# Kernel tuning notes

Hardware: AMD Instinct MI355X
Metric: run time of the kernel (lower is better)

The kernel has to match this reference:

```python
import jax, jax.numpy as jnp
import numpy as np

B, N = 2, 200
IMG = 2048
NC = 4                    # node concepts ('Is*')
NODE_CH = NC * 256        # 1024
EC = 3                    # edge concepts minus 'HigherPri'
AC = 4                    # actions
BBOX_MAX = 1024.0
E = N * (N - 1)

# static fully-connected directed edge list (src=i, dst=j, i!=j), row-major order
_ii, _jj = np.meshgrid(np.arange(N), np.arange(N), indexing='ij')
_m = _ii != _jj
SRC = jnp.asarray(_ii[_m])
DST = jnp.asarray(_jj[_m])


def _lin(k, fin, fout):
    kw, kb = jax.random.split(k)
    s = 1.0 / np.sqrt(fin)
    return (jax.random.uniform(kw, (fin, fout), jnp.float32, -s, s),
            jax.random.uniform(kb, (fout,), jnp.float32, -s, s))


def setup_inputs():
    ks = jax.random.split(jax.random.key(0), 16)
    p = {}
    p['roi_features'] = jax.random.normal(ks[0], (B, N, IMG), jnp.float32)
    p['batch_bboxes'] = jax.random.uniform(ks[1], (B, N, 4), jnp.float32) * BBOX_MAX
    p['batch_directions'] = jax.random.normal(ks[2], (B, N, 4), jnp.float32)
    p['batch_priorities'] = jax.random.normal(ks[3], (B, N), jnp.float32)
    p['w1'], p['b1'] = _lin(ks[4], IMG, 512)
    p['w2'], p['b2'] = _lin(ks[5], 512, 256)
    p['w3'], p['b3'] = _lin(ks[6], 256, NODE_CH)
    p['wi'], p['bi'] = _lin(ks[7], NODE_CH, NC)
    p['we1'], p['be1'] = _lin(ks[8], 16, 256)
    p['we2'], p['be2'] = _lin(ks[9], 256, 64)
    p['we3'], p['be3'] = _lin(ks[10], 64, EC)
    p['wp1'], p['bp1'] = _lin(ks[11], EC + 1, 128)
    p['wp2'], p['bp2'] = _lin(ks[12], 128, NODE_CH * AC)
    p['root_w'], _ = _lin(ks[13], NODE_CH, AC)
    _, p['root_b'] = _lin(ks[14], NODE_CH, AC)
    return p


def reference(roi_features, batch_bboxes, batch_directions, batch_priorities,
              w1, b1, w2, b2, w3, b3, wi, bi,
              we1, be1, we2, be2, we3, be3,
              wp1, bp1, wp2, bp2, root_w, root_b):
    # node concept embedding MLP: [B,N,IMG] -> [B,N,NODE_CH]
    h = jax.nn.relu(roi_features @ w1 + b1)
    h = jax.nn.relu(h @ w2 + b2)
    node_concepts = h @ w3 + b3
    node_concepts_explicit = jax.nn.sigmoid(node_concepts @ wi + bi)

    # pairwise attributes for all directed edges (same ordering as torch masks)
    node_attr = jnp.concatenate([batch_bboxes / BBOX_MAX, batch_directions], -1)  # [B,N,8]
    pair = jnp.concatenate([node_attr[:, SRC], node_attr[:, DST]], -1)            # [B,E,16]
    eh = jax.nn.relu(pair @ we1 + be1)
    eh = jax.nn.relu(eh @ we2 + be2)
    edge_attributes = jax.nn.sigmoid(eh @ we3 + be3)                              # [B,E,EC]
    higher_pri = (batch_priorities[:, SRC] > batch_priorities[:, DST]).astype(jnp.float32)
    edge_attributes = jnp.concatenate([edge_attributes, higher_pri[..., None]], -1)  # [B,E,EC+1]

    # NNConv on graph 0: per-edge weight matrix, gather-matmul-scatter
    x = node_concepts[0]                 # [N, NODE_CH]
    e = edge_attributes[0]               # [E, EC+1]
    w = jax.nn.relu(e @ wp1 + bp1) @ wp2 + bp2
    w = w.reshape(E, NODE_CH, AC)        # [E, NODE_CH, AC]
    msg = jnp.einsum('ei,eio->eo', x[SRC], w)          # [E, AC]
    agg = jax.ops.segment_sum(msg, DST, num_segments=N)  # [N, AC]
    next_actions = agg + x @ root_w + root_b
    return (next_actions, node_concepts_explicit[0], edge_attributes[0])
```

## Files before the change

kernel.cpp:

```cpp
#include <hip/hip_runtime.h>
#include <math.h>

#define NN 200
#define ETOT 39800

typedef float float4v __attribute__((ext_vector_type(4)));
typedef short short8 __attribute__((ext_vector_type(8)));

__device__ __forceinline__ float sigf(float x) { return 1.0f / (1.0f + expf(-x)); }

__device__ __forceinline__ unsigned short f2b(float f) {
  unsigned u = __float_as_uint(f);
  u += 0x7fffu + ((u >> 16) & 1u);
  return (unsigned short)(u >> 16);
}
__device__ __forceinline__ float b2f16(unsigned short u) {
  return __uint_as_float(((unsigned)u) << 16);
}

__global__ __launch_bounds__(256) void k_prep(
    const float* __restrict__ w1, const float* __restrict__ w2, const float* __restrict__ wp2,
    const float* __restrict__ w3, const float* __restrict__ wi, const float* __restrict__ rootw,
    const float* __restrict__ bp2, const float* __restrict__ b3, const float* __restrict__ we2,
    const float* __restrict__ bbox, const float* __restrict__ dir,
    const float* __restrict__ we1, const float* __restrict__ be1, const float* __restrict__ wp1,
    unsigned short* __restrict__ w1T, unsigned short* __restrict__ w2T,
    unsigned short* __restrict__ WrT, unsigned short* __restrict__ we2T,
    float* __restrict__ G12f, float* __restrict__ Pm, float* __restrict__ Qm,
    float* __restrict__ gvec, float* __restrict__ wp1T, float* __restrict__ bcat) {
  __shared__ __align__(16) char sm[16640];
  const int b = blockIdx.x, tid = threadIdx.x;
  const int lane = tid & 63, wv = tid >> 6;

  if (b < 288) {
    float (*lds)[65] = (float (*)[65])sm;
    const float* Wf;
    unsigned short* Wt;
    int K, N, t;
    if (b < 256) { Wf = w1; Wt = w1T; K = 2048; N = 512; t = b; }
    else { Wf = w2; Wt = w2T; K = 512; N = 256; t = b - 256; }
    const int K64 = K >> 6;
    const int kt = t % K64, nt = t / K64;
#pragma unroll 4
    for (int i = 0; i < 16; ++i) {
      int idx = tid + i * 256;
      int r = idx >> 6, c = idx & 63;
      lds[r][c] = Wf[(size_t)(kt * 64 + r) * N + nt * 64 + c];
    }
    __syncthreads();
#pragma unroll 4
    for (int i = 0; i < 16; ++i) {
      int idx = tid + i * 256;
      int r = idx >> 6, c = idx & 63;
      Wt[(size_t)(nt * 64 + r) * K + kt * 64 + c] = f2b(lds[c][r]);
    }
  } else if (b < 416) {
    int k = b - 288;
    int o = tid >> 6, l = tid & 63;
    const float* src = wp2 + (size_t)k * 4096;
    unsigned short* dst = WrT + (size_t)(k * 4 + o) * 1024;
    for (int i = l; i < 1024; i += 64) dst[i] = f2b(src[i * 4 + o]);
  } else if (b < 672) {
    const int c = b - 416;
    float s[12] = {};
#pragma unroll
    for (int ii = 0; ii < 4; ++ii) {
      int i = tid + ii * 256;
      float xv = w3[(size_t)c * 1024 + i];
      float4v wi4 = ((const float4v*)wi)[i];
      float4v rw4 = ((const float4v*)rootw)[i];
      float4v bp4 = ((const float4v*)bp2)[i];
#pragma unroll
      for (int q = 0; q < 4; ++q) {
        s[q] += xv * wi4[q]; s[4 + q] += xv * rw4[q]; s[8 + q] += xv * bp4[q];
      }
    }
    float (*part)[12] = (float (*)[12])sm;
#pragma unroll
    for (int r = 0; r < 12; ++r) {
      float v = s[r];
#pragma unroll
      for (int off = 32; off > 0; off >>= 1) v += __shfl_down(v, off, 64);
      if (lane == 0) part[wv][r] = v;
    }
    __syncthreads();
    if (tid < 12) G12f[c * 12 + tid] = part[0][tid] + part[1][tid] + part[2][tid] + part[3][tid];
  } else if (b < 872) {
    const int n = b - 672, c = tid;
    float a[8];
#pragma unroll
    for (int r = 0; r < 4; ++r) a[r] = bbox[n * 4 + r] * (1.0f / 1024.0f);
#pragma unroll
    for (int r = 0; r < 4; ++r) a[4 + r] = dir[n * 4 + r];
    float p = be1[c], q = 0.0f;
#pragma unroll
    for (int r = 0; r < 8; ++r) {
      p += a[r] * we1[r * 256 + c];
      q += a[r] * we1[(8 + r) * 256 + c];
    }
    Pm[n * 256 + c] = p;
    Qm[n * 256 + c] = q;
  } else if (b < 888) {
    const int f = (b - 872) * 256 + tid;
    const int c = f >> 6, k0 = (f & 63) * 4;
#pragma unroll
    for (int q = 0; q < 4; ++q)
      we2T[c * 256 + k0 + q] = f2b(we2[(k0 + q) * 64 + c]);
  } else if (b < 896) {
    const int j = (b - 888) * 64 + (tid >> 2), p = tid & 3;
    const float* src = wp2 + (size_t)(j >> 2) * 4096 + (j & 3);
    float v = 0.f;
    for (int t = 0; t < 256; ++t) {
      int i = p + 4 * t;
      v += b3[i] * src[4 * i];
    }
    v += __shfl_down(v, 2, 4);
    v += __shfl_down(v, 1, 4);
    if (p == 0) gvec[j] = v;
  } else if (b == 896) {
    if (tid < 128) {
      float4v v = {wp1[tid], wp1[128 + tid], wp1[256 + tid], wp1[384 + tid]};
      ((float4v*)wp1T)[tid] = v;
    }
  } else {
    float s[12] = {};
#pragma unroll
    for (int ii = 0; ii < 4; ++ii) {
      int i = tid + ii * 256;
      float xv = b3[i];
      float4v wi4 = ((const float4v*)wi)[i];
      float4v rw4 = ((const float4v*)rootw)[i];
      float4v bp4 = ((const float4v*)bp2)[i];
#pragma unroll
      for (int q = 0; q < 4; ++q) {
        s[q] += xv * wi4[q]; s[4 + q] += xv * rw4[q]; s[8 + q] += xv * bp4[q];
      }
    }
    float (*part)[12] = (float (*)[12])sm;
#pragma unroll
    for (int r = 0; r < 12; ++r) {
      float v = s[r];
#pragma unroll
      for (int off = 32; off > 0; off >>= 1) v += __shfl_down(v, off, 64);
      if (lane == 0) part[wv][r] = v;
    }
    __syncthreads();
    if (tid < 12) bcat[tid] = part[0][tid] + part[1][tid] + part[2][tid] + part[3][tid];
  }
}

__global__ __launch_bounds__(256) void k_mid(
    const float* __restrict__ roi, const unsigned short* __restrict__ w1T, const float* __restrict__ b1,
    const unsigned short* __restrict__ WrT, const float* __restrict__ w3,
    unsigned short* __restrict__ h1, unsigned short* __restrict__ Gm) {
  __shared__ float red[4][16][17];
  const int b = blockIdx.x, tid = threadIdx.x;
  const int lane = tid & 63, wv = tid >> 6, mr = lane & 15, quad = lane >> 4;

  if (b < 416) {
    const int m0 = (b % 13) * 16, n0 = (b / 13) * 16;
    const int arow = min(m0 + mr, 199);
    const float* Ap = roi + (size_t)arow * 2048 + wv * 512 + quad * 8;
    const unsigned short* Bp = w1T + (size_t)(n0 + mr) * 2048 + wv * 512 + quad * 8;
    float4v acc = {0.f, 0.f, 0.f, 0.f};
    for (int ks = 0; ks < 16; ++ks) {
      float4v a0 = *(const float4v*)(Ap + ks * 32);
      float4v a1 = *(const float4v*)(Ap + ks * 32 + 4);
      short8 af;
      af[0]=f2b(a0[0]); af[1]=f2b(a0[1]); af[2]=f2b(a0[2]); af[3]=f2b(a0[3]);
      af[4]=f2b(a1[0]); af[5]=f2b(a1[1]); af[6]=f2b(a1[2]); af[7]=f2b(a1[3]);
      short8 bf = *(const short8*)(Bp + ks * 32);
      acc = __builtin_amdgcn_mfma_f32_16x16x32_bf16(af, bf, acc, 0, 0, 0);
    }
#pragma unroll
    for (int r = 0; r < 4; ++r) red[wv][quad * 4 + r][mr] = acc[r];
    __syncthreads();
    const int row = tid >> 4, col = tid & 15;
    float v = red[0][row][col] + red[1][row][col] + red[2][row][col] + red[3][row][col] + b1[n0 + col];
    h1[(size_t)(m0 + row) * 512 + n0 + col] = f2b(fmaxf(v, 0.f));
  } else {
    const int t = b - 416;
    const int j0 = (t % 32) * 16, c0 = (t / 32) * 16;
    const unsigned short* Ap = WrT + (size_t)(j0 + mr) * 1024 + wv * 256 + quad * 8;
    const float* Bp = w3 + (size_t)(c0 + mr) * 1024 + wv * 256 + quad * 8;
    float4v acc = {0.f, 0.f, 0.f, 0.f};
    for (int ks = 0; ks < 8; ++ks) {
      short8 af = *(const short8*)(Ap + ks * 32);
      float4v b0 = *(const float4v*)(Bp + ks * 32);
      float4v b1v = *(const float4v*)(Bp + ks * 32 + 4);
      short8 bf;
      bf[0]=f2b(b0[0]); bf[1]=f2b(b0[1]); bf[2]=f2b(b0[2]); bf[3]=f2b(b0[3]);
      bf[4]=f2b(b1v[0]); bf[5]=f2b(b1v[1]); bf[6]=f2b(b1v[2]); bf[7]=f2b(b1v[3]);
      acc = __builtin_amdgcn_mfma_f32_16x16x32_bf16(af, bf, acc, 0, 0, 0);
    }
#pragma unroll
    for (int r = 0; r < 4; ++r) red[wv][quad * 4 + r][mr] = acc[r];
    __syncthreads();
    const int row = tid >> 4, col = tid & 15;
    float v = red[0][row][col] + red[1][row][col] + red[2][row][col] + red[3][row][col];
    Gm[(size_t)(j0 + row) * 256 + c0 + col] = f2b(v);
  }
}

__global__ __launch_bounds__(256) void k_h2(const unsigned short* __restrict__ h1,
                                            const unsigned short* __restrict__ w2T,
                                            const float* __restrict__ b2,
                                            unsigned short* __restrict__ h2) {
  __shared__ float red[4][16][17];
  const int tid = threadIdx.x, lane = tid & 63, wv = tid >> 6;
  const int m0 = (blockIdx.x % 13) * 16, n0 = (blockIdx.x / 13) * 16;
  const int mr = lane & 15, quad = lane >> 4;
  const unsigned short* Ap = h1 + (size_t)(m0 + mr) * 512 + wv * 128 + quad * 8;
  const unsigned short* Bp = w2T + (size_t)(n0 + mr) * 512 + wv * 128 + quad * 8;
  float4v acc = {0.f, 0.f, 0.f, 0.f};
#pragma unroll
  for (int s = 0; s < 4; ++s) {
    short8 af = *(const short8*)(Ap + s * 32);
    short8 bf = *(const short8*)(Bp + s * 32);
    acc = __builtin_amdgcn_mfma_f32_16x16x32_bf16(af, bf, acc, 0, 0, 0);
  }
#pragma unroll
  for (int r = 0; r < 4; ++r) red[wv][quad * 4 + r][mr] = acc[r];
  __syncthreads();
  const int row = tid >> 4, col = tid & 15;
  float v = red[0][row][col] + red[1][row][col] + red[2][row][col] + red[3][row][col] + b2[n0 + col];
  h2[(size_t)(m0 + row) * 256 + n0 + col] = f2b(fmaxf(v, 0.f));
}

__global__ __launch_bounds__(256) void k_TN(const unsigned short* __restrict__ h2,
                                            const unsigned short* __restrict__ Gm,
                                            const float* __restrict__ gvec,
                                            const float* __restrict__ G12f, const float* __restrict__ bcat,
                                            const float* __restrict__ bi, const float* __restrict__ rootb,
                                            float* __restrict__ Tm, float* __restrict__ out1,
                                            float* __restrict__ Um, float* __restrict__ out0) {
  __shared__ __align__(16) char sm[4352];
  const int b = blockIdx.x, tid = threadIdx.x;
  const int lane = tid & 63, wv = tid >> 6, mr = lane & 15, quad = lane >> 4;
  if (b < 416) {
    float (*red)[16][17] = (float (*)[16][17])sm;
    const int m0 = (b % 13) * 16, n0 = (b / 13) * 16;
    const unsigned short* Ap = h2 + (size_t)(m0 + mr) * 256 + wv * 64 + quad * 8;
    const unsigned short* Bp = Gm + (size_t)(n0 + mr) * 256 + wv * 64 + quad * 8;
    float4v acc = {0.f, 0.f, 0.f, 0.f};
#pragma unroll
    for (int s = 0; s < 2; ++s) {
      short8 af = *(const short8*)(Ap + s * 32);
      short8 bf = *(const short8*)(Bp + s * 32);
      acc = __builtin_amdgcn_mfma_f32_16x16x32_bf16(af, bf, acc, 0, 0, 0);
    }
#pragma unroll
    for (int r = 0; r < 4; ++r) red[wv][quad * 4 + r][mr] = acc[r];
    __syncthreads();
    const int row = tid >> 4, col = tid & 15;
    float v = red[0][row][col] + red[1][row][col] + red[2][row][col] + red[3][row][col] + gvec[n0 + col];
    Tm[(size_t)(m0 + row) * 512 + n0 + col] = v;
  } else {
    const int n = b - 416;
    const float xv = b2f16(h2[(size_t)n * 256 + tid]);
    const float4v* g4 = (const float4v*)(G12f + tid * 12);
    float s[12];
    float4v v0 = g4[0], v1 = g4[1], v2 = g4[2];
    s[0]=xv*v0[0]; s[1]=xv*v0[1]; s[2]=xv*v0[2]; s[3]=xv*v0[3];
    s[4]=xv*v1[0]; s[5]=xv*v1[1]; s[6]=xv*v1[2]; s[7]=xv*v1[3];
    s[8]=xv*v2[0]; s[9]=xv*v2[1]; s[10]=xv*v2[2]; s[11]=xv*v2[3];
    float (*part)[12] = (float (*)[12])sm;
#pragma unroll
    for (int r = 0; r < 12; ++r) {
      float v = s[r];
#pragma unroll
      for (int off = 32; off > 0; off >>= 1) v += __shfl_down(v, off, 64);
      if (lane == 0) part[wv][r] = v;
    }
    __syncthreads();
    if (tid < 12) {
      float v = part[0][tid] + part[1][tid] + part[2][tid] + part[3][tid] + bcat[tid];
      int kind = tid >> 2, c = tid & 3;
      if (kind == 0) out1[n * 4 + c] = sigf(v + bi[c]);
      else if (kind == 1) out0[n * 4 + c] = v + rootb[c];
      else Um[n * 4 + c] = v;
    }
  }
}

__global__ __launch_bounds__(256) void k_edge(
    const float* __restrict__ P, const float* __restrict__ Q,
    const unsigned short* __restrict__ we2T,
    const float* __restrict__ be2, const float* __restrict__ we3, const float* __restrict__ be3,
    const float* __restrict__ wp1T, const float* __restrict__ bp1,
    const float* __restrict__ pri,
    const float* __restrict__ T, const float* __restrict__ U,
    float* __restrict__ out0, float* __restrict__ out_ea) {
  __shared__ int src_s[64], dst_s[64];
  __shared__ float ea_s[64][4];
  __shared__ float4v wp1s[128];
  __shared__ float bp1s[128];
  __shared__ float4v Ts[2][128];
  __shared__ float Us[2][4];

  const int tid = threadIdx.x;
  const int e0 = blockIdx.x * 64;
  const int s_lo = e0 / 199;

  if (tid < 64) {
    int e = e0 + tid;
    int i = -1, j = 0;
    if (e < ETOT) {
      i = e / 199;
      int jj = e - i * 199;
      j = jj + (jj >= i ? 1 : 0);
    }
    src_s[tid] = i;
    dst_s[tid] = j;
  }
  if (tid < 128) {
    wp1s[tid] = ((const float4v*)wp1T)[tid];
    bp1s[tid] = bp1[tid];
  }
  {
    int row = tid >> 7, c = tid & 127;
    Ts[row][c] = ((const float4v*)T)[(s_lo + row) * 128 + c];
  }
  if (tid < 8) {
    int s = min(s_lo + (tid >> 2), 199);
    Us[tid >> 2][tid & 3] = U[s * 4 + (tid & 3)];
  }
  __syncthreads();

  const int lane = tid & 63;
  const int wv = tid >> 6;
  const int m = lane & 15;
  const int quad = lane >> 4;
  const int eloc = wv * 16 + m;
  const int si = src_s[eloc];
  const int dj = dst_s[eloc];

  float4v acc[4];
#pragma unroll
  for (int ct = 0; ct < 4; ++ct) { acc[ct][0] = 0.f; acc[ct][1] = 0.f; acc[ct][2] = 0.f; acc[ct][3] = 0.f; }

  const short8* W8 = (const short8*)we2T;

  for (int ks = 0; ks < 8; ++ks) {
    union { short8 s; unsigned u[4]; } af;
    af.s = (short8)0;
    if (si >= 0) {
      const float4v* p4 = (const float4v*)(P + si * 256 + ks * 32 + quad * 8);
      const float4v* q4 = (const float4v*)(Q + dj * 256 + ks * 32 + quad * 8);
      float4v v0 = p4[0] + q4[0];
      float4v v1 = p4[1] + q4[1];
      af.u[0] = (unsigned)f2b(fmaxf(v0[0], 0.f)) | ((unsigned)f2b(fmaxf(v0[1], 0.f)) << 16);
      af.u[1] = (unsigned)f2b(fmaxf(v0[2], 0.f)) | ((unsigned)f2b(fmaxf(v0[3], 0.f)) << 16);
      af.u[2] = (unsigned)f2b(fmaxf(v1[0], 0.f)) | ((unsigned)f2b(fmaxf(v1[1], 0.f)) << 16);
      af.u[3] = (unsigned)f2b(fmaxf(v1[2], 0.f)) | ((unsigned)f2b(fmaxf(v1[3], 0.f)) << 16);
    }
#pragma unroll
    for (int ct = 0; ct < 4; ++ct) {
      short8 bf = W8[(ct * 16 + m) * 32 + ks * 4 + quad];
      acc[ct] = __builtin_amdgcn_mfma_f32_16x16x32_bf16(af.s, bf, acc[ct], 0, 0, 0);
    }
  }

  float ev[4][3];
#pragma unroll
  for (int r = 0; r < 4; ++r) { ev[r][0] = 0.f; ev[r][1] = 0.f; ev[r][2] = 0.f; }
#pragma unroll
  for (int ct = 0; ct < 4; ++ct) {
    const int col = ct * 16 + m;
    const float b2v = be2[col];
    const float w0 = we3[col * 3 + 0], w1v = we3[col * 3 + 1], w2v = we3[col * 3 + 2];
#pragma unroll
    for (int r = 0; r < 4; ++r) {
      float e2 = fmaxf(acc[ct][r] + b2v, 0.f);
      ev[r][0] += e2 * w0;
      ev[r][1] += e2 * w1v;
      ev[r][2] += e2 * w2v;
    }
  }
#pragma unroll
  for (int r = 0; r < 4; ++r)
#pragma unroll
    for (int p = 0; p < 3; ++p) {
      float v = ev[r][p];
      v += __shfl_xor(v, 1, 64);
      v += __shfl_xor(v, 2, 64);
      v += __shfl_xor(v, 4, 64);
      v += __shfl_xor(v, 8, 64);
      ev[r][p] = v;
    }
  if (m == 0) {
#pragma unroll
    for (int r = 0; r < 4; ++r) {
      int el = wv * 16 + quad * 4 + r;
      int ss = src_s[el], dd = dst_s[el];
      if (ss >= 0) {
        float4v o;
        o[0] = sigf(ev[r][0] + be3[0]);
        o[1] = sigf(ev[r][1] + be3[1]);
        o[2] = sigf(ev[r][2] + be3[2]);
        o[3] = (pri[ss] > pri[dd]) ? 1.0f : 0.0f;
        *(float4v*)&ea_s[el][0] = o;
        *(float4v*)(out_ea + (size_t)(e0 + el) * 4) = o;
      }
    }
  }
  __syncthreads();

  const int ee = tid >> 2, pp = tid & 3;
  const int s2 = src_s[ee], d2 = dst_s[ee];
  float4v pm = {0.f, 0.f, 0.f, 0.f};
  if (s2 >= 0) {
    const int srow = s2 - s_lo;
    const float c0 = ea_s[ee][0], c1 = ea_s[ee][1], c2 = ea_s[ee][2], c3 = ea_s[ee][3];
#pragma unroll 8
    for (int tt = pp; tt < 128; tt += 4) {
      float4v w4 = wp1s[tt];
      float hv = bp1s[tt] + c0 * w4[0] + c1 * w4[1] + c2 * w4[2] + c3 * w4[3];
      hv = fmaxf(hv, 0.f);
      pm += hv * Ts[srow][tt];
    }
  }
#pragma unroll
  for (int o = 0; o < 4; ++o) {
    float v = pm[o];
    v += __shfl_xor(v, 1, 64);
    v += __shfl_xor(v, 2, 64);
    pm[o] = v;
  }
  if (s2 >= 0) atomicAdd(&out0[d2 * 4 + pp], Us[s2 - s_lo][pp] + pm[pp]);
}

extern "C" void kernel_launch(void* const* d_in, const int* in_sizes, int n_in,
                              void* d_out, int out_size, void* d_ws, size_t ws_size,
                              hipStream_t stream) {
  (void)in_sizes; (void)n_in; (void)out_size; (void)ws_size;
  const float* roi   = (const float*)d_in[0];
  const float* bbox  = (const float*)d_in[1];
  const float* dir   = (const float*)d_in[2];
  const float* pri   = (const float*)d_in[3];
  const float* w1    = (const float*)d_in[4];
  const float* b1    = (const float*)d_in[5];
  const float* w2    = (const float*)d_in[6];
  const float* b2    = (const float*)d_in[7];
  const float* w3    = (const float*)d_in[8];
  const float* b3    = (const float*)d_in[9];
  const float* wi    = (const float*)d_in[10];
  const float* bi    = (const float*)d_in[11];
  const float* we1   = (const float*)d_in[12];
  const float* be1   = (const float*)d_in[13];
  const float* we2   = (const float*)d_in[14];
  const float* be2   = (const float*)d_in[15];
  const float* we3   = (const float*)d_in[16];
  const float* be3   = (const float*)d_in[17];
  const float* wp1   = (const float*)d_in[18];
  const float* bp1   = (const float*)d_in[19];
  const float* wp2   = (const float*)d_in[20];
  const float* bp2   = (const float*)d_in[21];
  const float* rootw = (const float*)d_in[22];
  const float* rootb = (const float*)d_in[23];

  float* out0 = (float*)d_out;
  float* out1 = out0 + 800;
  float* out2 = out0 + 1600;

  unsigned short* us = (unsigned short*)d_ws;
  unsigned short* w1T  = us;
  unsigned short* w2T  = us + 1048576;
  unsigned short* WrT  = us + 1179648;
  unsigned short* we2T = us + 1703936;
  unsigned short* h1   = us + 1720320;
  unsigned short* h2   = us + 1826816;
  unsigned short* Gm   = us + 1880064;
  float* fb   = (float*)(us + 2011136);
  float* Tm   = fb;
  float* Pm   = fb + 106496;
  float* Qm   = fb + 157696;
  float* Um   = fb + 208896;
  float* wp1T = fb + 209696;
  float* G12f = fb + 210208;
  float* gvec = fb + 213280;
  float* bcat = fb + 213792;

  k_prep<<<898, 256, 0, stream>>>(w1, w2, wp2, w3, wi, rootw, bp2, b3, we2,
                                  bbox, dir, we1, be1, wp1,
                                  w1T, w2T, WrT, we2T, G12f, Pm, Qm, gvec, wp1T, bcat);

  k_mid<<<928, 256, 0, stream>>>(roi, w1T, b1, WrT, w3, h1, Gm);

  k_h2<<<208, 256, 0, stream>>>(h1, w2T, b2, h2);

  k_TN<<<616, 256, 0, stream>>>(h2, Gm, gvec, G12f, bcat, bi, rootb, Tm, out1, Um, out0);

  k_edge<<<622, 256, 0, stream>>>(Pm, Qm, we2T, be2, we3, be3, wp1T, bp1, pri, Tm, Um, out0, out2);
}
```

Baseline: 175.5 us.

## Fuse h2 layer computation into k_TN via shared-memory tile recompute

Removes the separate k_h2 launch: each k_TN block recomputes its 16-row h2 tile (h1 @ w2 + b2, relu) with MFMA into shared memory, then uses it for the Tm GEMM or the per-node 12-output reduction. The per-node branch now handles 16 nodes per block with 16-lane shuffles instead of one node per block, shrinking the grid from 616 to 429 blocks. This saves a kernel launch and the global h2 round trip, but each 16-row tile of h2 is recomputed by all 32 column blocks, which adds redundant MFMA work and w2T reads.

```diff
diff --git a/kernel.cpp b/kernel.cpp
--- a/kernel.cpp
+++ b/kernel.cpp
@@ -202,45 +202,44 @@
   }
 }
 
-__global__ __launch_bounds__(256) void k_h2(const unsigned short* __restrict__ h1,
+__global__ __launch_bounds__(256) void k_TN(const unsigned short* __restrict__ h1,
                                             const unsigned short* __restrict__ w2T,
                                             const float* __restrict__ b2,
-                                            unsigned short* __restrict__ h2) {
-  __shared__ float red[4][16][17];
-  const int tid = threadIdx.x, lane = tid & 63, wv = tid >> 6;
-  const int m0 = (blockIdx.x % 13) * 16, n0 = (blockIdx.x / 13) * 16;
-  const int mr = lane & 15, quad = lane >> 4;
-  const unsigned short* Ap = h1 + (size_t)(m0 + mr) * 512 + wv * 128 + quad * 8;
-  const unsigned short* Bp = w2T + (size_t)(n0 + mr) * 512 + wv * 128 + quad * 8;
-  float4v acc = {0.f, 0.f, 0.f, 0.f};
-#pragma unroll
-  for (int s = 0; s < 4; ++s) {
-    short8 af = *(const short8*)(Ap + s * 32);
-    short8 bf = *(const short8*)(Bp + s * 32);
-    acc = __builtin_amdgcn_mfma_f32_16x16x32_bf16(af, bf, acc, 0, 0, 0);
-  }
-#pragma unroll
-  for (int r = 0; r < 4; ++r) red[wv][quad * 4 + r][mr] = acc[r];
-  __syncthreads();
-  const int row = tid >> 4, col = tid & 15;
-  float v = red[0][row][col] + red[1][row][col] + red[2][row][col] + red[3][row][col] + b2[n0 + col];
-  h2[(size_t)(m0 + row) * 256 + n0 + col] = f2b(fmaxf(v, 0.f));
-}
-
-__global__ __launch_bounds__(256) void k_TN(const unsigned short* __restrict__ h2,
                                             const unsigned short* __restrict__ Gm,
                                             const float* __restrict__ gvec,
                                             const float* __restrict__ G12f, const float* __restrict__ bcat,
                                             const float* __restrict__ bi, const float* __restrict__ rootb,
                                             float* __restrict__ Tm, float* __restrict__ out1,
                                             float* __restrict__ Um, float* __restrict__ out0) {
-  __shared__ __align__(16) char sm[4352];
+  __shared__ unsigned short h2s[16 * 264];
+  __shared__ float red[4][16][17];
   const int b = blockIdx.x, tid = threadIdx.x;
   const int lane = tid & 63, wv = tid >> 6, mr = lane & 15, quad = lane >> 4;
+
+  const int m0 = (b < 416) ? (b % 13) * 16 : (b - 416) * 16;
+
+#pragma unroll
+  for (int ct = 0; ct < 4; ++ct) {
+    const int n2 = wv * 64 + ct * 16;
+    const unsigned short* Ap = h1 + (size_t)(m0 + mr) * 512 + quad * 8;
+    const unsigned short* Bp = w2T + (size_t)(n2 + mr) * 512 + quad * 8;
+    float4v acc = {0.f, 0.f, 0.f, 0.f};
+#pragma unroll
+    for (int ks = 0; ks < 16; ++ks) {
+      short8 af = *(const short8*)(Ap + ks * 32);
+      short8 bf = *(const short8*)(Bp + ks * 32);
+      acc = __builtin_amdgcn_mfma_f32_16x16x32_bf16(af, bf, acc, 0, 0, 0);
+    }
+    const float b2v = b2[n2 + mr];
+#pragma unroll
+    for (int r = 0; r < 4; ++r)
+      h2s[(quad * 4 + r) * 264 + n2 + mr] = f2b(fmaxf(acc[r] + b2v, 0.f));
+  }
+  __syncthreads();
+
   if (b < 416) {
-    float (*red)[16][17] = (float (*)[16][17])sm;
-    const int m0 = (b % 13) * 16, n0 = (b / 13) * 16;
-    const unsigned short* Ap = h2 + (size_t)(m0 + mr) * 256 + wv * 64 + quad * 8;
+    const int n0 = (b / 13) * 16;
+    const unsigned short* Ap = h2s + mr * 264 + wv * 64 + quad * 8;
     const unsigned short* Bp = Gm + (size_t)(n0 + mr) * 256 + wv * 64 + quad * 8;
     float4v acc = {0.f, 0.f, 0.f, 0.f};
 #pragma unroll
@@ -256,29 +255,32 @@
     float v = red[0][row][col] + red[1][row][col] + red[2][row][col] + red[3][row][col] + gvec[n0 + col];
     Tm[(size_t)(m0 + row) * 512 + n0 + col] = v;
   } else {
-    const int n = b - 416;
-    const float xv = b2f16(h2[(size_t)n * 256 + tid]);
-    const float4v* g4 = (const float4v*)(G12f + tid * 12);
-    float s[12];
-    float4v v0 = g4[0], v1 = g4[1], v2 = g4[2];
-    s[0]=xv*v0[0]; s[1]=xv*v0[1]; s[2]=xv*v0[2]; s[3]=xv*v0[3];
-    s[4]=xv*v1[0]; s[5]=xv*v1[1]; s[6]=xv*v1[2]; s[7]=xv*v1[3];
-    s[8]=xv*v2[0]; s[9]=xv*v2[1]; s[10]=xv*v2[2]; s[11]=xv*v2[3];
-    float (*part)[12] = (float (*)[12])sm;
+    const int nl = tid >> 4;
+    const int cp = tid & 15;
+    float s[12] = {};
+#pragma unroll 4
+    for (int q = 0; q < 16; ++q) {
+      const int c = cp * 16 + q;
+      const float xv = b2f16(h2s[nl * 264 + c]);
+      const float* g = G12f + c * 12;
+#pragma unroll
+      for (int r = 0; r < 12; ++r) s[r] += xv * g[r];
+    }
 #pragma unroll
     for (int r = 0; r < 12; ++r) {
-      float v = s[r];
-#pragma unroll
-      for (int off = 32; off > 0; off >>= 1) v += __shfl_down(v, off, 64);
-      if (lane == 0) part[wv][r] = v;
-    }
-    __syncthreads();
-    if (tid < 12) {
-      float v = part[0][tid] + part[1][tid] + part[2][tid] + part[3][tid] + bcat[tid];
-      int kind = tid >> 2, c = tid & 3;
-      if (kind == 0) out1[n * 4 + c] = sigf(v + bi[c]);
-      else if (kind == 1) out0[n * 4 + c] = v + rootb[c];
-      else Um[n * 4 + c] = v;
+      s[r] += __shfl_down(s[r], 8, 16);
+      s[r] += __shfl_down(s[r], 4, 16);
+      s[r] += __shfl_down(s[r], 2, 16);
+      s[r] += __shfl_down(s[r], 1, 16);
+    }
+    const int n = m0 + nl;
+    if (cp == 0 && n < NN) {
+#pragma unroll
+      for (int c = 0; c < 4; ++c) {
+        out1[n * 4 + c] = sigf(s[c] + bcat[c] + bi[c]);
+        out0[n * 4 + c] = s[4 + c] + bcat[4 + c] + rootb[c];
+        Um[n * 4 + c] = s[8 + c] + bcat[8 + c];
+      }
     }
   }
 }
@@ -469,7 +471,6 @@
   unsigned short* WrT  = us + 1179648;
   unsigned short* we2T = us + 1703936;
   unsigned short* h1   = us + 1720320;
-  unsigned short* h2   = us + 1826816;
   unsigned short* Gm   = us + 1880064;
   float* fb   = (float*)(us + 2011136);
   float* Tm   = fb;
@@ -487,9 +488,8 @@
 
   k_mid<<<928, 256, 0, stream>>>(roi, w1T, b1, WrT, w3, h1, Gm);
 
-  k_h2<<<208, 256, 0, stream>>>(h1, w2T, b2, h2);
-
-  k_TN<<<616, 256, 0, stream>>>(h2, Gm, gvec, G12f, bcat, bi, rootb, Tm, out1, Um, out0);
+  k_TN<<<429, 256, 0, stream>>>(h1, w2T, b2, Gm, gvec, G12f, bcat, bi, rootb,
+                                Tm, out1, Um, out0);
 
   k_edge<<<622, 256, 0, stream>>>(Pm, Qm, we2T, be2, we3, be3, wp1T, bp1, pri, Tm, Um, out0, out2);
 }
```

Result: slower. 202.4 us (+15.4%).
